# Kernel tuning notes

Hardware: AMD Instinct MI355X
Metric: run time of the kernel (lower is better)

The kernel has to match this reference:

```python
import jax, jax.numpy as jnp
import numpy as np

NUM_HEADS = 8
LN_EPS = 1e-5


def _layernorm(x, g, b):
    mu = jnp.mean(x, axis=-1, keepdims=True)
    var = jnp.mean((x - mu) ** 2, axis=-1, keepdims=True)
    return (x - mu) * jax.lax.rsqrt(var + LN_EPS) * g + b


def setup_inputs() -> dict:
    key = jax.random.key(0)
    B, T, N, D = 16, 12, 325, 128
    F = 256
    ks = jax.random.split(key, 16)
    s = 0.02
    return {
        "x": jax.random.normal(ks[0], (B, T, N, D), dtype=jnp.float32),
        "Wq": jax.random.normal(ks[1], (D, D), dtype=jnp.float32) * s,
        "bq": jnp.zeros((D,), jnp.float32),
        "Wk": jax.random.normal(ks[2], (D, D), dtype=jnp.float32) * s,
        "bk": jnp.zeros((D,), jnp.float32),
        "Wv": jax.random.normal(ks[3], (D, D), dtype=jnp.float32) * s,
        "bv": jnp.zeros((D,), jnp.float32),
        "Wo": jax.random.normal(ks[4], (D, D), dtype=jnp.float32) * s,
        "bo": jnp.zeros((D,), jnp.float32),
        "ln1_g": jnp.ones((D,), jnp.float32),
        "ln1_b": jnp.zeros((D,), jnp.float32),
        "W1": jax.random.normal(ks[5], (D, F), dtype=jnp.float32) * s,
        "b1": jnp.zeros((F,), jnp.float32),
        "W2": jax.random.normal(ks[6], (F, D), dtype=jnp.float32) * s,
        "b2": jnp.zeros((D,), jnp.float32),
        "ln2_g": jnp.ones((D,), jnp.float32),
        "ln2_b": jnp.zeros((D,), jnp.float32),
    }


def reference(x, Wq, bq, Wk, bk, Wv, bv, Wo, bo, ln1_g, ln1_b, W1, b1, W2, b2, ln2_g, ln2_b):
    B, T, N, D = x.shape
    H = NUM_HEADS
    hd = D // H
    # Conv2d 1x1 projections == per-channel linear over last dim
    q = (x @ Wq + bq).reshape(B, T, N, H, hd)
    k = (x @ Wk + bk).reshape(B, T, N, H, hd)
    v = (x @ Wv + bv).reshape(B, T, N, H, hd)
    # attention across the node dim (n,m), per (batch, head, time)
    scores = jnp.einsum("btnhd,btmhd->bhtnm", q, k) / jnp.sqrt(jnp.float32(hd))
    attn = jax.nn.softmax(scores, axis=-1)
    out = jnp.einsum("bhtnm,btmhd->btnhd", attn, v).reshape(B, T, N, D)
    out = out @ Wo + bo
    out = _layernorm(x + out, ln1_g, ln1_b)
    ffn = jax.nn.gelu(out @ W1 + b1, approximate=False) @ W2 + b2
    return _layernorm(out + ffn, ln2_g, ln2_b)
```

## Files before the change

kernel.cpp:

```cpp
#include <hip/hip_runtime.h>
#include <hip/hip_bf16.h>
#include <math.h>

#define B_ 16
#define T_ 12
#define N_ 325
#define D_ 128
#define H_ 8
#define HD_ 16
#define F_ 256
#define ROWS (B_*T_*N_)
#define NP 336
#define QK_STRIDE 20
#define VT_STRIDE 340
#define LN_EPS 1e-5f

typedef __hip_bfloat16 bf16;
typedef __attribute__((ext_vector_type(8))) short bf16x8;
typedef __attribute__((ext_vector_type(4))) short bf16x4;
typedef __attribute__((ext_vector_type(4))) float f32x4;

__device__ __forceinline__ float b2f(bf16 v) { return __bfloat162float(v); }
__device__ __forceinline__ bf16  f2b(float v) { return __float2bfloat16(v); }

__device__ __forceinline__ float fexp2(float v) { return __builtin_amdgcn_exp2f(v); }
__device__ __forceinline__ float frcp(float v) { return __builtin_amdgcn_rcpf(v); }

union frag_cvt  { uint4 u; bf16x8 s; };
union frag4_cvt { uint2 u; bf16x4 s; };
union h2u       { __hip_bfloat162 h; unsigned u; };

__device__ __forceinline__ bf16x8 frag_ld(const void* p) {
    frag_cvt c; c.u = *(const uint4*)p; return c.s;
}
__device__ __forceinline__ bf16x4 frag4_ld(const void* p) {
    frag4_cvt c; c.u = *(const uint2*)p; return c.s;
}

__device__ __forceinline__ unsigned pk2(float a, float b) {
    h2u c; c.h = __float22bfloat162_rn(make_float2(a, b)); return c.u;
}

__device__ __forceinline__ bf16x4 pack4_rtn(f32x4 v) {
    frag4_cvt c;
    c.u.x = pk2(v[0], v[1]);
    c.u.y = pk2(v[2], v[3]);
    return c.s;
}

__device__ __forceinline__ bf16x8 pack8_rtn(float4 a, float4 b) {
    frag_cvt c;
    c.u.x = pk2(a.x, a.y);
    c.u.y = pk2(a.z, a.w);
    c.u.z = pk2(b.x, b.y);
    c.u.w = pk2(b.z, b.w);
    return c.s;
}

__device__ __forceinline__ float gelu_fast(float a) {
    float z = fexp2(2.3022083f * a * (1.f + 0.044715f * a * a));
    return a * z * frcp(z + 1.f);
}

#define MFMA16(a_, b_, c_) __builtin_amdgcn_mfma_f32_16x16x16bf16_1k((a_), (b_), (c_), 0, 0, 0)
#define MFMA32(a_, b_, c_) __builtin_amdgcn_mfma_f32_16x16x32_bf16((a_), (b_), (c_), 0, 0, 0)

__global__ void convert_weights(const float* __restrict__ Wq, const float* __restrict__ Wk,
                                const float* __restrict__ Wv, const float* __restrict__ Wo,
                                const float* __restrict__ W1, const float* __restrict__ W2,
                                bf16* __restrict__ wt) {
    int i = blockIdx.x * 256 + threadIdx.x;
    if (i < 16384)       { int k = i >> 7, n = i & 127;                    wt[n * 128 + k] = f2b(Wq[i]); }
    else if (i < 32768)  { int j = i - 16384; int k = j >> 7, n = j & 127; wt[16384 + n * 128 + k] = f2b(Wk[j]); }
    else if (i < 49152)  { int j = i - 32768; int k = j >> 7, n = j & 127; wt[32768 + n * 128 + k] = f2b(Wv[j]); }
    else if (i < 65536)  { int j = i - 49152; int k = j >> 7, n = j & 127;
                           wt[49152 + n * 128 + (k ^ ((n & 7) << 3))] = f2b(Wo[j]); }
    else if (i < 98304)  { int j = i - 65536; int k = j >> 8, n = j & 255;
                           wt[65536 + n * 128 + (k ^ ((n & 7) << 3))] = f2b(W1[j]); }
    else                 { int j = i - 98304; int k = j >> 7, n = j & 127;
                           wt[98304 + n * 256 + (k ^ ((n & 7) << 3))] = f2b(W2[j]); }
}

__global__ __launch_bounds__(256) void qkv_attn_kernel(
        const float* __restrict__ x, const bf16* __restrict__ wt,
        const float* __restrict__ bq, const float* __restrict__ bk,
        const float* __restrict__ bv, bf16* __restrict__ ao) {
    __shared__ __align__(16) bf16 qsh[NP * QK_STRIDE];
    __shared__ __align__(16) bf16 ksh[NP * QK_STRIDE];
    __shared__ __align__(16) bf16 vsh_t[HD_ * VT_STRIDE];

    int bid  = blockIdx.x;
    int bt   = bid % 192;
    int h    = bid / 192;
    int tid  = threadIdx.x;
    int wave = tid >> 6;
    int lane = tid & 63;
    int lm   = lane & 15;
    int quad = lane >> 4;

    bf16x8 bfrag[3][4];
    #pragma unroll
    for (int mat = 0; mat < 3; mat++) {
        const bf16* Wt = wt + mat * 16384 + (size_t)(h * 16 + lm) * 128;
        #pragma unroll
        for (int ks = 0; ks < 4; ks++)
            bfrag[mat][ks] = frag_ld(Wt + ks * 32 + quad * 8);
    }
    float bqv = bq[h * 16 + lm], bkv = bk[h * 16 + lm], bvv = bv[h * 16 + lm];
    const float QSCALE = 0.25f * 1.44269504f;

    const float* xslab = x + (size_t)bt * N_ * D_;
    for (int mt = wave; mt < 21; mt += 4) {
        int row  = mt * 16 + lm;
        int crow = row < N_ ? row : N_ - 1;
        const float* xr = xslab + (size_t)crow * D_;
        bf16x8 af[4];
        #pragma unroll
        for (int ks = 0; ks < 4; ks++) {
            const float4* p = (const float4*)(xr + ks * 32 + quad * 8);
            af[ks] = pack8_rtn(p[0], p[1]);
        }
        f32x4 cq = {0.f,0.f,0.f,0.f}, ck = {0.f,0.f,0.f,0.f}, cv = {0.f,0.f,0.f,0.f};
        #pragma unroll
        for (int ks = 0; ks < 4; ks++) {
            cq = MFMA32(af[ks], bfrag[0][ks], cq);
            ck = MFMA32(af[ks], bfrag[1][ks], ck);
            cv = MFMA32(af[ks], bfrag[2][ks], cv);
        }
        #pragma unroll
        for (int reg = 0; reg < 4; reg++) {
            int r = mt * 16 + quad * 4 + reg;
            bool v = r < N_;
            qsh[r * QK_STRIDE + lm]  = f2b(v ? (cq[reg] + bqv) * QSCALE : 0.f);
            ksh[r * QK_STRIDE + lm]  = f2b(v ? (ck[reg] + bkv) : 0.f);
            vsh_t[lm * VT_STRIDE + r] = f2b(v ? (cv[reg] + bvv) : 0.f);
        }
    }
    __syncthreads();

    const f32x4 zero = {0.f, 0.f, 0.f, 0.f};
    for (int qt0 = wave; qt0 < 21; qt0 += 8) {
        int qt1  = qt0 + 4;
        int qt1c = qt1 < 21 ? qt1 : 20;
        bf16x4 qf0 = frag4_ld(qsh + (qt0  * 16 + lm) * QK_STRIDE + quad * 4);
        bf16x4 qf1 = frag4_ld(qsh + (qt1c * 16 + lm) * QK_STRIDE + quad * 4);
        f32x4 o0 = zero, o1 = zero;
        float L0 = 0.f, L1 = 0.f;
        for (int kt = 0; kt < 20; kt++) {
            bf16x4 kf = frag4_ld(ksh + (kt * 16 + lm) * QK_STRIDE + quad * 4);
            bf16x4 vf = frag4_ld(vsh_t + lm * VT_STRIDE + kt * 16 + quad * 4);
            f32x4 s0 = MFMA16(kf, qf0, zero);
            f32x4 s1 = MFMA16(kf, qf1, zero);
            f32x4 p0, p1;
            p0[0] = fexp2(s0[0]); p0[1] = fexp2(s0[1]);
            p0[2] = fexp2(s0[2]); p0[3] = fexp2(s0[3]);
            p1[0] = fexp2(s1[0]); p1[1] = fexp2(s1[1]);
            p1[2] = fexp2(s1[2]); p1[3] = fexp2(s1[3]);
            L0 += (p0[0] + p0[1]) + (p0[2] + p0[3]);
            L1 += (p1[0] + p1[1]) + (p1[2] + p1[3]);
            o0 = MFMA16(vf, pack4_rtn(p0), o0);
            o1 = MFMA16(vf, pack4_rtn(p1), o1);
        }
        {
            bf16x4 kf = frag4_ld(ksh + (20 * 16 + lm) * QK_STRIDE + quad * 4);
            bf16x4 vf = frag4_ld(vsh_t + lm * VT_STRIDE + 20 * 16 + quad * 4);
            f32x4 s0 = MFMA16(kf, qf0, zero);
            f32x4 s1 = MFMA16(kf, qf1, zero);
            f32x4 p0, p1;
            #pragma unroll
            for (int reg = 0; reg < 4; reg++) {
                bool ok = (quad * 4 + reg) < 5;
                p0[reg] = ok ? fexp2(s0[reg]) : 0.f;
                p1[reg] = ok ? fexp2(s1[reg]) : 0.f;
            }
            L0 += (p0[0] + p0[1]) + (p0[2] + p0[3]);
            L1 += (p1[0] + p1[1]) + (p1[2] + p1[3]);
            o0 = MFMA16(vf, pack4_rtn(p0), o0);
            o1 = MFMA16(vf, pack4_rtn(p1), o1);
        }
        L0 += __shfl_xor(L0, 16, 64); L0 += __shfl_xor(L0, 32, 64);
        L1 += __shfl_xor(L1, 16, 64); L1 += __shfl_xor(L1, 32, 64);
        float i0 = frcp(L0), i1 = frcp(L1);
        int n0 = qt0 * 16 + lm;
        if (n0 < N_) {
            frag4_cvt o;
            o.u.x = pk2(o0[0] * i0, o0[1] * i0);
            o.u.y = pk2(o0[2] * i0, o0[3] * i0);
            *(uint2*)(ao + ((size_t)bt * N_ + n0) * D_ + h * HD_ + quad * 4) = o.u;
        }
        int n1 = qt1 * 16 + lm;
        if (qt1 < 21 && n1 < N_) {
            frag4_cvt o;
            o.u.x = pk2(o1[0] * i1, o1[1] * i1);
            o.u.y = pk2(o1[2] * i1, o1[3] * i1);
            *(uint2*)(ao + ((size_t)bt * N_ + n1) * D_ + h * HD_ + quad * 4) = o.u;
        }
    }
}

#define US_STRIDE 136
#define H_STRIDE  264

__global__ __launch_bounds__(256) void epilogue_mfma(
        const float* __restrict__ x, const bf16* __restrict__ ao,
        const bf16* __restrict__ wt,
        const float* __restrict__ bo,
        const float* __restrict__ g1, const float* __restrict__ be1,
        const float* __restrict__ fb1, const float* __restrict__ fb2,
        const float* __restrict__ g2, const float* __restrict__ be2,
        float* __restrict__ out) {
    __shared__ __align__(16) bf16 bufA[16384];
    __shared__ __align__(16) bf16 bufB[16384];
    __shared__ __align__(16) bf16 bufC[16384];
    __shared__ __align__(16) bf16 us_lds[4][16 * US_STRIDE];
    __shared__ __align__(16) bf16 h_lds[4][16 * H_STRIDE];

    const bf16* Wot = wt + 49152;
    const bf16* W1t = wt + 65536;
    const bf16* W2t = wt + 98304;

    int tid  = threadIdx.x;
    int wave = tid >> 6;
    int lm   = tid & 15;
    int quad = (tid & 63) >> 4;
    int r0   = blockIdx.x * 64 + wave * 16;
    int sw   = (lm & 7) << 3;

    bf16* us = us_lds[wave];
    bf16* hh = h_lds[wave];

    bf16x8 afrag[8];

    {
        const bf16* ar = ao + (size_t)(r0 + lm) * D_;
        #pragma unroll
        for (int ks = 0; ks < 4; ks++)
            afrag[ks] = frag_ld(ar + ks * 32 + quad * 8);
    }

    {
        const uint4* gs0 = (const uint4*)Wot;
        const uint4* gs1 = (const uint4*)W1t;
        uint4* lA = (uint4*)bufA;
        uint4* lB = (uint4*)bufB;
        #pragma unroll
        for (int i = 0; i < 8; i++) lA[tid + i * 256] = gs0[tid + i * 256];
        #pragma unroll
        for (int i = 0; i < 8; i++) lB[tid + i * 256] = gs1[tid + i * 256];
    }
    __syncthreads();

    f32x4 acc[8];
    #pragma unroll
    for (int nt = 0; nt < 8; nt++) {
        f32x4 c = {0.f, 0.f, 0.f, 0.f};
        const bf16* w = bufA + (size_t)(nt * 16 + lm) * 128;
        #pragma unroll
        for (int ks = 0; ks < 4; ks++) {
            bf16x8 b = frag_ld(w + ((ks * 32 + quad * 8) ^ sw));
            c = MFMA32(afrag[ks], b, c);
        }
        acc[nt] = c;
    }

    float bov[8], g1v[8], be1v[8], g2v[8], be2v[8], fb2v[8];
    #pragma unroll
    for (int nt = 0; nt < 8; nt++) {
        int col = nt * 16 + lm;
        bov[nt] = bo[col]; g1v[nt] = g1[col]; be1v[nt] = be1[col];
        g2v[nt] = g2[col]; be2v[nt] = be2[col]; fb2v[nt] = fb2[col];
    }
    float usv[8][4];
    #pragma unroll
    for (int rg = 0; rg < 4; rg++) {
        int grow = r0 + quad * 4 + rg;
        const float* xr = x + (size_t)grow * D_;
        float rr[8];
        float s = 0.f, s2 = 0.f;
        #pragma unroll
        for (int nt = 0; nt < 8; nt++) {
            rr[nt] = acc[nt][rg] + bov[nt] + xr[nt * 16 + lm];
            s += rr[nt]; s2 += rr[nt] * rr[nt];
        }
        #pragma unroll
        for (int mk = 1; mk < 16; mk <<= 1) {
            s += __shfl_xor(s, mk, 64); s2 += __shfl_xor(s2, mk, 64);
        }
        float mu  = s * (1.f / 128.f);
        float var = s2 * (1.f / 128.f) - mu * mu;
        float rstd = rsqrtf(var + LN_EPS);
        int lrow = quad * 4 + rg;
        #pragma unroll
        for (int nt = 0; nt < 8; nt++) {
            float u = (rr[nt] - mu) * rstd * g1v[nt] + be1v[nt];
            usv[nt][rg] = u;
            us[lrow * US_STRIDE + nt * 16 + lm] = f2b(u);
        }
    }
    {
        const uint4* gs = ((const uint4*)W1t) + 2048;
        uint4* lC = (uint4*)bufC;
        #pragma unroll
        for (int i = 0; i < 8; i++) lC[tid + i * 256] = gs[tid + i * 256];
    }
    __syncthreads();

    #pragma unroll
    for (int ks = 0; ks < 4; ks++)
        afrag[ks] = frag_ld(&us[lm * US_STRIDE + ks * 32 + quad * 8]);
    #pragma unroll
    for (int nt = 0; nt < 8; nt++) {
        f32x4 c = {0.f, 0.f, 0.f, 0.f};
        const bf16* w = bufB + (size_t)(nt * 16 + lm) * 128;
        #pragma unroll
        for (int ks = 0; ks < 4; ks++) {
            bf16x8 b = frag_ld(w + ((ks * 32 + quad * 8) ^ sw));
            c = MFMA32(afrag[ks], b, c);
        }
        int col = nt * 16 + lm;
        float fb = fb1[col];
        #pragma unroll
        for (int rg = 0; rg < 4; rg++) {
            float hg = gelu_fast(c[rg] + fb);
            hh[(quad * 4 + rg) * H_STRIDE + col] = f2b(hg);
        }
    }
    #pragma unroll
    for (int nt = 8; nt < 16; nt++) {
        f32x4 c = {0.f, 0.f, 0.f, 0.f};
        const bf16* w = bufC + (size_t)((nt - 8) * 16 + lm) * 128;
        #pragma unroll
        for (int ks = 0; ks < 4; ks++) {
            bf16x8 b = frag_ld(w + ((ks * 32 + quad * 8) ^ sw));
            c = MFMA32(afrag[ks], b, c);
        }
        int col = nt * 16 + lm;
        float fb = fb1[col];
        #pragma unroll
        for (int rg = 0; rg < 4; rg++) {
            float hg = gelu_fast(c[rg] + fb);
            hh[(quad * 4 + rg) * H_STRIDE + col] = f2b(hg);
        }
    }
    {
        const uint4* gs = (const uint4*)W2t;
        uint4* lA = (uint4*)bufA;
        #pragma unroll
        for (int i = 0; i < 8; i++) lA[tid + i * 256] = gs[tid + i * 256];
    }
    __syncthreads();

    #pragma unroll
    for (int ks = 0; ks < 8; ks++)
        afrag[ks] = frag_ld(&hh[lm * H_STRIDE + ks * 32 + quad * 8]);
    #pragma unroll
    for (int nt = 0; nt < 4; nt++) {
        f32x4 c = {0.f, 0.f, 0.f, 0.f};
        const bf16* w = bufA + (size_t)(nt * 16 + lm) * 256;
        #pragma unroll
        for (int ks = 0; ks < 8; ks++) {
            bf16x8 b = frag_ld(w + ((ks * 32 + quad * 8) ^ sw));
            c = MFMA32(afrag[ks], b, c);
        }
        acc[nt] = c;
    }
    {
        const uint4* gs = ((const uint4*)W2t) + 2048;
        uint4* lB = (uint4*)bufB;
        #pragma unroll
        for (int i = 0; i < 8; i++) lB[tid + i * 256] = gs[tid + i * 256];
    }
    __syncthreads();

    #pragma unroll
    for (int nt = 4; nt < 8; nt++) {
        f32x4 c = {0.f, 0.f, 0.f, 0.f};
        const bf16* w = bufB + (size_t)((nt - 4) * 16 + lm) * 256;
        #pragma unroll
        for (int ks = 0; ks < 8; ks++) {
            bf16x8 b = frag_ld(w + ((ks * 32 + quad * 8) ^ sw));
            c = MFMA32(afrag[ks], b, c);
        }
        acc[nt] = c;
    }
    #pragma unroll
    for (int rg = 0; rg < 4; rg++) {
        float yy[8];
        float s = 0.f, s2 = 0.f;
        #pragma unroll
        for (int nt = 0; nt < 8; nt++) {
            yy[nt] = acc[nt][rg] + fb2v[nt] + usv[nt][rg];
            s += yy[nt]; s2 += yy[nt] * yy[nt];
        }
        #pragma unroll
        for (int mk = 1; mk < 16; mk <<= 1) {
            s += __shfl_xor(s, mk, 64); s2 += __shfl_xor(s2, mk, 64);
        }
        float mu  = s * (1.f / 128.f);
        float var = s2 * (1.f / 128.f) - mu * mu;
        float rstd = rsqrtf(var + LN_EPS);
        int grow = r0 + quad * 4 + rg;
        float* orow = out + (size_t)grow * D_;
        #pragma unroll
        for (int nt = 0; nt < 8; nt++)
            orow[nt * 16 + lm] = (yy[nt] - mu) * rstd * g2v[nt] + be2v[nt];
    }
}

extern "C" void kernel_launch(void* const* d_in, const int* in_sizes, int n_in,
                              void* d_out, int out_size, void* d_ws, size_t ws_size,
                              hipStream_t stream) {
    const float* x   = (const float*)d_in[0];
    const float* Wq  = (const float*)d_in[1];
    const float* bq  = (const float*)d_in[2];
    const float* Wk  = (const float*)d_in[3];
    const float* bk  = (const float*)d_in[4];
    const float* Wv  = (const float*)d_in[5];
    const float* bv  = (const float*)d_in[6];
    const float* Wo  = (const float*)d_in[7];
    const float* bo  = (const float*)d_in[8];
    const float* g1  = (const float*)d_in[9];
    const float* be1 = (const float*)d_in[10];
    const float* W1  = (const float*)d_in[11];
    const float* fb1 = (const float*)d_in[12];
    const float* W2  = (const float*)d_in[13];
    const float* fb2 = (const float*)d_in[14];
    const float* g2  = (const float*)d_in[15];
    const float* be2 = (const float*)d_in[16];
    float* out = (float*)d_out;

    bf16* wt = (bf16*)d_ws;
    bf16* ao = wt + 131072;

    convert_weights<<<512, 256, 0, stream>>>(Wq, Wk, Wv, Wo, W1, W2, wt);
    qkv_attn_kernel<<<B_ * T_ * H_, 256, 0, stream>>>(x, wt, bq, bk, bv, ao);
    epilogue_mfma<<<ROWS / 64, 256, 0, stream>>>(x, ao, wt, bo, g1, be1, fb1, fb2,
                                                 g2, be2, out);
}
```

Before: 205.9 us.

## Split fused epilogue into two kernels to cut LDS footprint

Replaces the single fused epilogue (out-projection, LN1, FFN, LN2) with two kernels. The first writes the LN1 output to a global bf16 scratch buffer, and the second runs the FFN and LN2 while reading that buffer back. Each kernel uses one 32KB weight buffer, restaged in halves for W1 and W2, instead of three, which lowers LDS use and should allow more blocks per CU. The cost is an extra global round-trip of the intermediate activation, an extra launch, and more barriers. The split path only runs if the workspace is large enough.

Result: no change. 202.8 us (-1.5%).

```diff
diff --git a/kernel.cpp b/kernel.cpp
--- a/kernel.cpp
+++ b/kernel.cpp
@@ -201,6 +201,232 @@
 #define US_STRIDE 136
 #define H_STRIDE  264
 
+__global__ __launch_bounds__(256) void epi_a(
+        const float* __restrict__ x, const bf16* __restrict__ ao,
+        const bf16* __restrict__ wt, const float* __restrict__ bo,
+        const float* __restrict__ g1, const float* __restrict__ be1,
+        bf16* __restrict__ usg) {
+    __shared__ __align__(16) bf16 wbuf[16384];
+
+    const bf16* Wot = wt + 49152;
+    int tid  = threadIdx.x;
+    int wave = tid >> 6;
+    int lm   = tid & 15;
+    int quad = (tid & 63) >> 4;
+    int r0   = blockIdx.x * 64 + wave * 16;
+    int sw   = (lm & 7) << 3;
+
+    bf16x8 afrag[4];
+    {
+        const bf16* ar = ao + (size_t)(r0 + lm) * D_;
+        #pragma unroll
+        for (int ks = 0; ks < 4; ks++)
+            afrag[ks] = frag_ld(ar + ks * 32 + quad * 8);
+    }
+    {
+        const uint4* gs = (const uint4*)Wot;
+        uint4*       ls = (uint4*)wbuf;
+        #pragma unroll
+        for (int i = 0; i < 8; i++) ls[tid + i * 256] = gs[tid + i * 256];
+    }
+    __syncthreads();
+
+    f32x4 acc[8];
+    #pragma unroll
+    for (int nt = 0; nt < 8; nt++) {
+        f32x4 c = {0.f, 0.f, 0.f, 0.f};
+        const bf16* w = wbuf + (size_t)(nt * 16 + lm) * 128;
+        #pragma unroll
+        for (int ks = 0; ks < 4; ks++) {
+            bf16x8 b = frag_ld(w + ((ks * 32 + quad * 8) ^ sw));
+            c = MFMA32(afrag[ks], b, c);
+        }
+        acc[nt] = c;
+    }
+
+    float bov[8], g1v[8], be1v[8];
+    #pragma unroll
+    for (int nt = 0; nt < 8; nt++) {
+        int col = nt * 16 + lm;
+        bov[nt] = bo[col]; g1v[nt] = g1[col]; be1v[nt] = be1[col];
+    }
+    #pragma unroll
+    for (int rg = 0; rg < 4; rg++) {
+        int grow = r0 + quad * 4 + rg;
+        const float* xr = x + (size_t)grow * D_;
+        float rr[8];
+        float s = 0.f, s2 = 0.f;
+        #pragma unroll
+        for (int nt = 0; nt < 8; nt++) {
+            rr[nt] = acc[nt][rg] + bov[nt] + xr[nt * 16 + lm];
+            s += rr[nt]; s2 += rr[nt] * rr[nt];
+        }
+        #pragma unroll
+        for (int mk = 1; mk < 16; mk <<= 1) {
+            s += __shfl_xor(s, mk, 64); s2 += __shfl_xor(s2, mk, 64);
+        }
+        float mu  = s * (1.f / 128.f);
+        float var = s2 * (1.f / 128.f) - mu * mu;
+        float rstd = rsqrtf(var + LN_EPS);
+        bf16* ur = usg + (size_t)grow * D_;
+        #pragma unroll
+        for (int nt = 0; nt < 8; nt++)
+            ur[nt * 16 + lm] = f2b((rr[nt] - mu) * rstd * g1v[nt] + be1v[nt]);
+    }
+}
+
+__global__ __launch_bounds__(256) void epi_b(
+        const bf16* __restrict__ usg, const bf16* __restrict__ wt,
+        const float* __restrict__ fb1, const float* __restrict__ fb2,
+        const float* __restrict__ g2, const float* __restrict__ be2,
+        float* __restrict__ out) {
+    __shared__ __align__(16) bf16 wbuf[16384];
+    __shared__ __align__(16) bf16 h_lds[4][16 * H_STRIDE];
+
+    const bf16* W1t = wt + 65536;
+    const bf16* W2t = wt + 98304;
+
+    int tid  = threadIdx.x;
+    int wave = tid >> 6;
+    int lm   = tid & 15;
+    int quad = (tid & 63) >> 4;
+    int r0   = blockIdx.x * 64 + wave * 16;
+    int sw   = (lm & 7) << 3;
+
+    bf16* hh = h_lds[wave];
+    bf16x8 afrag[8];
+
+    {
+        const bf16* ur = usg + (size_t)(r0 + lm) * D_;
+        #pragma unroll
+        for (int ks = 0; ks < 4; ks++)
+            afrag[ks] = frag_ld(ur + ks * 32 + quad * 8);
+    }
+    {
+        const uint4* gs = (const uint4*)W1t;
+        uint4*       ls = (uint4*)wbuf;
+        #pragma unroll
+        for (int i = 0; i < 8; i++) ls[tid + i * 256] = gs[tid + i * 256];
+    }
+    __syncthreads();
+
+    #pragma unroll
+    for (int nt = 0; nt < 8; nt++) {
+        f32x4 c = {0.f, 0.f, 0.f, 0.f};
+        const bf16* w = wbuf + (size_t)(nt * 16 + lm) * 128;
+        #pragma unroll
+        for (int ks = 0; ks < 4; ks++) {
+            bf16x8 b = frag_ld(w + ((ks * 32 + quad * 8) ^ sw));
+            c = MFMA32(afrag[ks], b, c);
+        }
+        int col = nt * 16 + lm;
+        float fb = fb1[col];
+        #pragma unroll
+        for (int rg = 0; rg < 4; rg++)
+            hh[(quad * 4 + rg) * H_STRIDE + col] = f2b(gelu_fast(c[rg] + fb));
+    }
+    __syncthreads();
+
+    {
+        const uint4* gs = ((const uint4*)W1t) + 2048;
+        uint4*       ls = (uint4*)wbuf;
+        #pragma unroll
+        for (int i = 0; i < 8; i++) ls[tid + i * 256] = gs[tid + i * 256];
+    }
+    __syncthreads();
+
+    #pragma unroll
+    for (int nt = 8; nt < 16; nt++) {
+        f32x4 c = {0.f, 0.f, 0.f, 0.f};
+        const bf16* w = wbuf + (size_t)((nt - 8) * 16 + lm) * 128;
+        #pragma unroll
+        for (int ks = 0; ks < 4; ks++) {
+            bf16x8 b = frag_ld(w + ((ks * 32 + quad * 8) ^ sw));
+            c = MFMA32(afrag[ks], b, c);
+        }
+        int col = nt * 16 + lm;
+        float fb = fb1[col];
+        #pragma unroll
+        for (int rg = 0; rg < 4; rg++)
+            hh[(quad * 4 + rg) * H_STRIDE + col] = f2b(gelu_fast(c[rg] + fb));
+    }
+    __syncthreads();
+
+    #pragma unroll
+    for (int ks = 0; ks < 8; ks++)
+        afrag[ks] = frag_ld(&hh[lm * H_STRIDE + ks * 32 + quad * 8]);
+    {
+        const uint4* gs = (const uint4*)W2t;
+        uint4*       ls = (uint4*)wbuf;
+        #pragma unroll
+        for (int i = 0; i < 8; i++) ls[tid + i * 256] = gs[tid + i * 256];
+    }
+    __syncthreads();
+
+    f32x4 acc[8];
+    #pragma unroll
+    for (int nt = 0; nt < 4; nt++) {
+        f32x4 c = {0.f, 0.f, 0.f, 0.f};
+        const bf16* w = wbuf + (size_t)(nt * 16 + lm) * 256;
+        #pragma unroll
+        for (int ks = 0; ks < 8; ks++) {
+            bf16x8 b = frag_ld(w + ((ks * 32 + quad * 8) ^ sw));
+            c = MFMA32(afrag[ks], b, c);
+        }
+        acc[nt] = c;
+    }
+    __syncthreads();
+
+    {
+        const uint4* gs = ((const uint4*)W2t) + 2048;
+        uint4*       ls = (uint4*)wbuf;
+        #pragma unroll
+        for (int i = 0; i < 8; i++) ls[tid + i * 256] = gs[tid + i * 256];
+    }
+    __syncthreads();
+
+    #pragma unroll
+    for (int nt = 4; nt < 8; nt++) {
+        f32x4 c = {0.f, 0.f, 0.f, 0.f};
+        const bf16* w = wbuf + (size_t)((nt - 4) * 16 + lm) * 256;
+        #pragma unroll
+        for (int ks = 0; ks < 8; ks++) {
+            bf16x8 b = frag_ld(w + ((ks * 32 + quad * 8) ^ sw));
+            c = MFMA32(afrag[ks], b, c);
+        }
+        acc[nt] = c;
+    }
+    float fb2v[8], g2v[8], be2v[8];
+    #pragma unroll
+    for (int nt = 0; nt < 8; nt++) {
+        int col = nt * 16 + lm;
+        fb2v[nt] = fb2[col]; g2v[nt] = g2[col]; be2v[nt] = be2[col];
+    }
+    #pragma unroll
+    for (int rg = 0; rg < 4; rg++) {
+        int grow = r0 + quad * 4 + rg;
+        const bf16* ur = usg + (size_t)grow * D_;
+        float yy[8];
+        float s = 0.f, s2 = 0.f;
+        #pragma unroll
+        for (int nt = 0; nt < 8; nt++) {
+            yy[nt] = acc[nt][rg] + fb2v[nt] + b2f(ur[nt * 16 + lm]);
+            s += yy[nt]; s2 += yy[nt] * yy[nt];
+        }
+        #pragma unroll
+        for (int mk = 1; mk < 16; mk <<= 1) {
+            s += __shfl_xor(s, mk, 64); s2 += __shfl_xor(s2, mk, 64);
+        }
+        float mu  = s * (1.f / 128.f);
+        float var = s2 * (1.f / 128.f) - mu * mu;
+        float rstd = rsqrtf(var + LN_EPS);
+        float* orow = out + (size_t)grow * D_;
+        #pragma unroll
+        for (int nt = 0; nt < 8; nt++)
+            orow[nt * 16 + lm] = (yy[nt] - mu) * rstd * g2v[nt] + be2v[nt];
+    }
+}
+
 __global__ __launch_bounds__(256) void epilogue_mfma(
         const float* __restrict__ x, const bf16* __restrict__ ao,
         const bf16* __restrict__ wt,
@@ -230,14 +456,12 @@
     bf16* hh = h_lds[wave];
 
     bf16x8 afrag[8];
-
     {
         const bf16* ar = ao + (size_t)(r0 + lm) * D_;
         #pragma unroll
         for (int ks = 0; ks < 4; ks++)
             afrag[ks] = frag_ld(ar + ks * 32 + quad * 8);
     }
-
     {
         const uint4* gs0 = (const uint4*)Wot;
         const uint4* gs1 = (const uint4*)W1t;
@@ -262,7 +486,6 @@
         }
         acc[nt] = c;
     }
-
     float bov[8], g1v[8], be1v[8], g2v[8], be2v[8], fb2v[8];
     #pragma unroll
     for (int nt = 0; nt < 8; nt++) {
@@ -320,10 +543,8 @@
         int col = nt * 16 + lm;
         float fb = fb1[col];
         #pragma unroll
-        for (int rg = 0; rg < 4; rg++) {
-            float hg = gelu_fast(c[rg] + fb);
-            hh[(quad * 4 + rg) * H_STRIDE + col] = f2b(hg);
-        }
+        for (int rg = 0; rg < 4; rg++)
+            hh[(quad * 4 + rg) * H_STRIDE + col] = f2b(gelu_fast(c[rg] + fb));
     }
     #pragma unroll
     for (int nt = 8; nt < 16; nt++) {
@@ -337,10 +558,8 @@
         int col = nt * 16 + lm;
         float fb = fb1[col];
         #pragma unroll
-        for (int rg = 0; rg < 4; rg++) {
-            float hg = gelu_fast(c[rg] + fb);
-            hh[(quad * 4 + rg) * H_STRIDE + col] = f2b(hg);
-        }
+        for (int rg = 0; rg < 4; rg++)
+            hh[(quad * 4 + rg) * H_STRIDE + col] = f2b(gelu_fast(c[rg] + fb));
     }
     {
         const uint4* gs = (const uint4*)W2t;
@@ -429,11 +648,19 @@
     const float* be2 = (const float*)d_in[16];
     float* out = (float*)d_out;
 
-    bf16* wt = (bf16*)d_ws;
-    bf16* ao = wt + 131072;
+    bf16* wt  = (bf16*)d_ws;
+    bf16* ao  = wt + 131072;
+    bf16* usg = ao + (size_t)ROWS * D_;
+    const size_t need_split = (size_t)(131072 + 2 * (size_t)ROWS * D_) * sizeof(bf16);
+    bool split = ws_size >= need_split;
 
     convert_weights<<<512, 256, 0, stream>>>(Wq, Wk, Wv, Wo, W1, W2, wt);
     qkv_attn_kernel<<<B_ * T_ * H_, 256, 0, stream>>>(x, wt, bq, bk, bv, ao);
-    epilogue_mfma<<<ROWS / 64, 256, 0, stream>>>(x, ao, wt, bo, g1, be1, fb1, fb2,
-                                                 g2, be2, out);
-}
+    if (split) {
+        epi_a<<<ROWS / 64, 256, 0, stream>>>(x, ao, wt, bo, g1, be1, usg);
+        epi_b<<<ROWS / 64, 256, 0, stream>>>(usg, wt, fb1, fb2, g2, be2, out);
+    } else {
+        epilogue_mfma<<<ROWS / 64, 256, 0, stream>>>(x, ao, wt, bo, g1, be1, fb1,
+                                                     fb2, g2, be2, out);
+    }
+}
```
